# Kernel optimization log

Hardware: AMD Instinct MI355X
Metric: run time of the kernel (lower is better)

## Reference

```python
import jax, jax.numpy as jnp
import numpy as np


def _dct2(x):
    """DCT-II over last dim, scipy norm=None scaling (matches the torch rfft trick:
    X_k = 2 * sum_n x_n cos(pi*k*(2n+1)/(2N))). Expressed as one batched matmul."""
    N = x.shape[-1]
    n = jnp.arange(N, dtype=x.dtype)
    k = jnp.arange(N, dtype=x.dtype)
    # D[k, n] = 2*cos(pi*k*(2n+1)/(2N))
    D = 2.0 * jnp.cos((np.pi / (2.0 * N)) * k[:, None] * (2.0 * n[None, :] + 1.0))
    return jnp.einsum('kn,bcn->bck', D, x)


def setup_inputs() -> dict:
    key = jax.random.key(0)
    k0, k1, k2 = jax.random.split(key, 3)
    b, c, l = 32, 512, 1024
    x = jax.random.normal(k0, (b, c, l), dtype=jnp.float32)
    # 1x1 Conv1d weights (kernel_size=1, bias=False) stored as [out, in]
    w1 = jax.random.normal(k1, (2 * c, c), dtype=jnp.float32) / np.float32(np.sqrt(c))
    w2 = jax.random.normal(k2, (c, 2 * c), dtype=jnp.float32) / np.float32(np.sqrt(2 * c))
    ln_w = jnp.ones((l,), dtype=jnp.float32)
    ln_b = jnp.zeros((l,), dtype=jnp.float32)
    return {"x": x, "w1": w1, "w2": w2, "ln_w": ln_w, "ln_b": ln_b}


def reference(x, w1, w2, ln_w, ln_b):
    eps = 1e-6
    freq = _dct2(x)                                   # [b, c, l]
    mu = jnp.mean(freq, axis=-1, keepdims=True)
    var = jnp.var(freq, axis=-1, keepdims=True)       # biased, like nn.LayerNorm
    h = (freq - mu) * jax.lax.rsqrt(var + eps) * ln_w + ln_b
    # fc: Conv1d(c->2c, k=1) -> Dropout(eval: identity) -> ReLU -> Conv1d(2c->c) -> Sigmoid
    h = jax.nn.relu(jnp.einsum('oi,bil->bol', w1, h))  # [b, 2c, l]
    gate = jax.nn.sigmoid(jnp.einsum('oi,bil->bol', w2, h))  # [b, c, l]
    return x * gate
```

## Files before the change

### kernel.cpp

```cpp
#include <hip/hip_runtime.h>
#include <hip/hip_bf16.h>
#include <math.h>

typedef short short8 __attribute__((ext_vector_type(8)));
typedef short short4v __attribute__((ext_vector_type(4)));
typedef float f32x4 __attribute__((ext_vector_type(4)));

__device__ __forceinline__ short f2bf(float f) {
  union { float f; unsigned u; } v; v.f = f;
  unsigned r = v.u + 0x7FFFu + ((v.u >> 16) & 1u);
  return (short)(r >> 16);
}
__device__ __forceinline__ float bf2f(short s) {
  union { unsigned u; float f; } v; v.u = ((unsigned)(unsigned short)s) << 16;
  return v.f;
}

__global__ __launch_bounds__(256) void cast_kernel(const float* __restrict__ in,
                                                   short* __restrict__ out, int n4) {
  int i = blockIdx.x * blockDim.x + threadIdx.x;
  if (i < n4) {
    float4 v = ((const float4*)in)[i];
    short4v o;
    o.x = f2bf(v.x); o.y = f2bf(v.y); o.z = f2bf(v.z); o.w = f2bf(v.w);
    ((short4v*)out)[i] = o;
  }
}

__global__ __launch_bounds__(256) void prep_eo(const float* __restrict__ x,
                                               short* __restrict__ eo) {
  int t = blockIdx.x * 256 + threadIdx.x;
  int bc = t >> 7, n0 = (t & 127) * 4;
  const float* xr = x + (size_t)bc * 1024;
  float4 f = *(const float4*)(xr + n0);
  float4 r = *(const float4*)(xr + 1020 - n0);
  short4v ef, of;
  ef.x = f2bf(f.x + r.w); ef.y = f2bf(f.y + r.z); ef.z = f2bf(f.z + r.y); ef.w = f2bf(f.w + r.x);
  of.x = f2bf(f.x - r.w); of.y = f2bf(f.y - r.z); of.z = f2bf(f.z - r.y); of.w = f2bf(f.w - r.x);
  *(short4v*)&eo[(size_t)bc * 512 + n0] = ef;
  *(short4v*)&eo[8388608 + (size_t)bc * 512 + n0] = of;
}

__global__ __launch_bounds__(256) void build_Deo(short* __restrict__ D) {
  int t = blockIdx.x * 256 + threadIdx.x;
  int parity = t >> 18, rem = t & 262143;
  int k2 = rem >> 9, n = rem & 511;
  const float s = 1.5339807878856412e-03f;
  float arg = (s * (float)(2 * k2 + parity)) * (float)(2 * n + 1);
  D[t] = f2bf(2.0f * cosf(arg));
}

__global__ __launch_bounds__(256) void ln_stats(const float2* __restrict__ partial,
                                                float2* __restrict__ musd) {
  int n = blockIdx.x * 256 + threadIdx.x;
  float S = 0.f, Q = 0.f;
#pragma unroll
  for (int r = 0; r < 4; ++r) {
    float2 p = partial[(size_t)r * 16384 + n];
    S += p.x; Q += p.y;
  }
  float mu  = S * (1.f / 1024.f);
  float var = Q * (1.f / 1024.f) - mu * mu;
  float2 o; o.x = mu; o.y = rsqrtf(var + 1e-6f);
  musd[n] = o;
}

__global__ __launch_bounds__(256) void ln_apply(short* __restrict__ freqT,
                                                const float2* __restrict__ musd,
                                                const float* __restrict__ lnw,
                                                const float* __restrict__ lnb) {
  int t = blockIdx.x * 256 + threadIdx.x;
  int c8 = t & 63;
  int k  = (t >> 6) & 1023;
  int b  = t >> 16;
  size_t idx = ((size_t)b << 19) + (size_t)k * 512 + (size_t)c8 * 8;
  short8 v = *(const short8*)&freqT[idx];
  float w  = lnw[k];
  float bb = lnb[k];
  const float2* ms = &musd[b * 512 + c8 * 8];
  short8 o;
#pragma unroll
  for (int j = 0; j < 8; ++j) {
    float f = bf2f(v[j]);
    float2 m = ms[j];
    o[j] = f2bf((f - m.x) * m.y * w + bb);
  }
  *(short8*)&freqT[idx] = o;
}

template<int EPI>
__global__ __launch_bounds__(256, 2) void gemmF(
    const short* __restrict__ A, const short* __restrict__ B,
    void* __restrict__ Cout, const float* __restrict__ X,
    float2* __restrict__ P, int K, int NT, long strideA, long strideB)
{
  __shared__ short As[2][8192];
  __shared__ short Bs[2][4096];
  const int tid = threadIdx.x;
  const int l   = tid & 63;
  const int w   = tid >> 6;
  const int wm  = w >> 1;
  const int wc  = w & 1;
  const int lr  = l & 15;
  const int lhi = l >> 4;

  const int nwg = gridDim.x, q = nwg >> 3, orig = blockIdx.x;
  const int wgid = (orig & 7) * q + (orig >> 3);
  int bx, by, bz;
  if (EPI == 0)      { bx = wgid & 1; bz = (wgid >> 1) & 1; by = wgid >> 2; }
  else if (EPI == 1) { by = wgid & 7; bx = (wgid >> 3) & 3; bz = wgid >> 5; }
  else               { bx = wgid & 1; by = (wgid >> 1) & 7; bz = wgid >> 4; }

  const long row0 = (long)bx * 256, col0 = (long)by * 128;
  const short* Ab = A + (size_t)bz * strideA + (size_t)row0 * K;
  const short* Bb = B + (size_t)bz * strideB + (size_t)col0 * K;

  const int sx    = (lhi ^ ((lr >> 1) & 3)) * 8;
  const int abase = (wm * 128 + lr) * 32;
  const int bbase = (wc * 64  + lr) * 32;

  f32x4 acc[8][4];
#pragma unroll
  for (int i = 0; i < 8; ++i)
#pragma unroll
    for (int j = 0; j < 4; ++j) acc[i][j] = (f32x4){0.f, 0.f, 0.f, 0.f};

#define GLL(SRC, DST) __builtin_amdgcn_global_load_lds(                      \
      (const __attribute__((address_space(1))) void*)(SRC),                  \
      (__attribute__((address_space(3))) void*)(DST), 16, 0, 0)

#define STAGE(KT, D) do {                                                    \
    const size_t kb_ = (size_t)(KT) * 32;                                    \
    _Pragma("unroll")                                                        \
    for (int r_ = 0; r_ < 4; ++r_) {                                         \
      int c_ = r_ * 256 + tid; int row_ = c_ >> 2; int sl_ = c_ & 3;         \
      int sc_ = (sl_ ^ ((row_ >> 1) & 3)) * 8;                               \
      GLL(Ab + (size_t)row_ * K + kb_ + sc_, &As[D][row_ * 32 + sl_ * 8]);   \
    }                                                                        \
    _Pragma("unroll")                                                        \
    for (int r_ = 0; r_ < 2; ++r_) {                                         \
      int c_ = r_ * 256 + tid; int row_ = c_ >> 2; int sl_ = c_ & 3;         \
      int sc_ = (sl_ ^ ((row_ >> 1) & 3)) * 8;                               \
      GLL(Bb + (size_t)row_ * K + kb_ + sc_, &Bs[D][row_ * 32 + sl_ * 8]);   \
    }                                                                        \
  } while (0)

#define LD8(PTR, OFF) (*(const short8*)&(PTR)[OFF])
#define MFMA(AV, BV, C) __builtin_amdgcn_mfma_f32_16x16x32_bf16(AV, BV, C, 0, 0, 0)
#define SBAR __builtin_amdgcn_s_barrier()
#define SCHB __builtin_amdgcn_sched_barrier(0)

#define MROW(MI, AV)                                                         \
    acc[MI][0] = MFMA(AV, b0, acc[MI][0]);                                   \
    acc[MI][1] = MFMA(AV, b1, acc[MI][1]);                                   \
    acc[MI][2] = MFMA(AV, b2, acc[MI][2]);                                   \
    acc[MI][3] = MFMA(AV, b3, acc[MI][3]);

  STAGE(0, 0);
  STAGE(1, 1);

  int cur = 0;
  for (int kt = 0; kt < NT; ++kt) {
    if (kt + 1 < NT) { asm volatile("s_waitcnt vmcnt(6)" ::: "memory"); }
    else             { asm volatile("s_waitcnt vmcnt(0)" ::: "memory"); }
    SCHB; SBAR;
    const short* Ad = As[cur];
    const short* Bd = Bs[cur];
    short8 a0, a1, a2, a3, a4, a5, a6, a7, b0, b1, b2, b3;
    a0 = LD8(Ad, abase + 0 * 512 + sx);
    a1 = LD8(Ad, abase + 1 * 512 + sx);
    b0 = LD8(Bd, bbase + 0 * 512 + sx);
    b1 = LD8(Bd, bbase + 1 * 512 + sx);
    b2 = LD8(Bd, bbase + 2 * 512 + sx);
    b3 = LD8(Bd, bbase + 3 * 512 + sx);
    a2 = LD8(Ad, abase + 2 * 512 + sx);
    a3 = LD8(Ad, abase + 3 * 512 + sx);
    a4 = LD8(Ad, abase + 4 * 512 + sx);
    a5 = LD8(Ad, abase + 5 * 512 + sx);
    a6 = LD8(Ad, abase + 6 * 512 + sx);
    a7 = LD8(Ad, abase + 7 * 512 + sx);
    SCHB;
    asm volatile("s_waitcnt lgkmcnt(6)" ::: "memory");
    SCHB;
    __builtin_amdgcn_s_setprio(1);
    MROW(0, a0) MROW(1, a1)
    __builtin_amdgcn_s_setprio(0);
    SCHB;
    asm volatile("s_waitcnt lgkmcnt(0)" ::: "memory");
    SCHB; SBAR;
    if (kt + 2 < NT) STAGE(kt + 2, cur);
    SCHB;
    __builtin_amdgcn_s_setprio(1);
    MROW(2, a2) MROW(3, a3) MROW(4, a4) MROW(5, a5) MROW(6, a6) MROW(7, a7)
    __builtin_amdgcn_s_setprio(0);
    SCHB;
    cur ^= 1;
  }

  float sv[4], qv[4];
#pragma unroll
  for (int ni = 0; ni < 4; ++ni) { sv[ni] = 0.f; qv[ni] = 0.f; }

#pragma unroll
  for (int mi = 0; mi < 8; ++mi) {
#pragma unroll
    for (int ni = 0; ni < 4; ++ni) {
#pragma unroll
      for (int j = 0; j < 4; ++j) {
        int r  = (int)row0 + wm * 128 + mi * 16 + lhi * 4 + j;
        int cc = (int)col0 + wc * 64 + ni * 16 + lr;
        float v = acc[mi][ni][j];
        if (EPI == 0) {
          sv[ni] += v; qv[ni] += v * v;
          int rr = r * 2 + bz;
          ((short*)Cout)[((size_t)(cc >> 9) << 19) + (size_t)rr * 512 + (cc & 511)] = f2bf(v);
        } else if (EPI == 1) {
          ((short*)Cout)[(size_t)bz * 1048576 + (size_t)r * 1024 + cc] = f2bf(v > 0.f ? v : 0.f);
        } else {
          size_t idx = (size_t)bz * 524288 + (size_t)r * 1024 + cc;
          float g = 1.f / (1.f + __expf(-v));
          ((float*)Cout)[idx] = X[idx] * g;
        }
      }
    }
  }

  if (EPI == 0) {
    __syncthreads();
    float* redS = (float*)&As[0][0];
    float* redQ = redS + 1024;
    const int contrib = wm * 4 + lhi;
#pragma unroll
    for (int ni = 0; ni < 4; ++ni) {
      int ccl = wc * 64 + ni * 16 + lr;
      redS[ccl * 8 + contrib] = sv[ni];
      redQ[ccl * 8 + contrib] = qv[ni];
    }
    __syncthreads();
    if (tid < 128) {
      float S = 0.f, Q = 0.f;
#pragma unroll
      for (int i = 0; i < 8; ++i) { S += redS[tid * 8 + i]; Q += redQ[tid * 8 + i]; }
      float2 o; o.x = S; o.y = Q;
      P[(size_t)(bz * 2 + bx) * 16384 + col0 + tid] = o;
    }
  }
#undef MROW
#undef MFMA
#undef LD8
#undef STAGE
#undef GLL
#undef SBAR
#undef SCHB
}

extern "C" void kernel_launch(void* const* d_in, const int* in_sizes, int n_in,
                              void* d_out, int out_size, void* d_ws, size_t ws_size,
                              hipStream_t stream) {
  const float* x    = (const float*)d_in[0];
  const float* w1   = (const float*)d_in[1];
  const float* w2   = (const float*)d_in[2];
  const float* ln_w = (const float*)d_in[3];
  const float* ln_b = (const float*)d_in[4];
  float* out = (float*)d_out;

  char* ws = (char*)d_ws;
  short* Deo    = (short*)(ws);
  short* w1_bf  = (short*)(ws + 1048576);
  short* w2_bf  = (short*)(ws + 2097152);
  short* freqT  = (short*)(ws + 3145728);
  short* z1t    = (short*)(ws + 36700160);
  short* eo     = z1t;
  float2* part  = (float2*)(ws + 103809024);
  float2* musd  = (float2*)(ws + 104857600);

  prep_eo<<<dim3(8192), dim3(256), 0, stream>>>(x, eo);
  cast_kernel<<<dim3(512), dim3(256), 0, stream>>>(w1, w1_bf, 524288 / 4);
  cast_kernel<<<dim3(512), dim3(256), 0, stream>>>(w2, w2_bf, 524288 / 4);
  build_Deo<<<dim3(2048), dim3(256), 0, stream>>>(Deo);

  gemmF<0><<<dim3(512), dim3(256), 0, stream>>>(
      Deo, eo, (void*)freqT, nullptr, part, 512, 16, 262144, 8388608);

  ln_stats<<<dim3(64), dim3(256), 0, stream>>>(part, musd);

  ln_apply<<<dim3(8192), dim3(256), 0, stream>>>(freqT, musd, ln_w, ln_b);

  gemmF<1><<<dim3(1024), dim3(256), 0, stream>>>(
      freqT, w1_bf, (void*)z1t, nullptr, nullptr, 512, 16, 524288, 0);

  gemmF<2><<<dim3(512), dim3(256), 0, stream>>>(
      w2_bf, z1t, (void*)out, x, nullptr, 1024, 32, 0, 1048576);
}
```

Measured before the change: 159.1 us.

## Compute LayerNorm stats analytically from input and fuse normalize into DCT GEMM epilogue

Computes the DCT-domain mean as a dot product of x with a precomputed column-sum vector, and the variance through Parseval-style identities on x. This moves the statistics into prep_eo and lets the first GEMM epilogue apply LayerNorm directly. It removes the partial-stat reduction, the ln_stats kernel and the separate ln_apply read-modify-write pass over the bf16 freq tensor. In exchange it adds two tiny kernels that build the cosine-sum vector, and stats computed in fp32 from x rather than from the bf16-rounded GEMM output.

```diff
diff --git a/kernel.cpp b/kernel.cpp
--- a/kernel.cpp
+++ b/kernel.cpp
@@ -27,8 +27,27 @@
   }
 }
 
+__global__ __launch_bounds__(256) void vbuild(float* __restrict__ vpart) {
+  int t = blockIdx.x * 256 + threadIdx.x;
+  int n = t & 1023, ch = t >> 10;
+  float coef = 1.5339807878856412e-03f * (float)(2 * n + 1);
+  float s = 0.f;
+  for (int k = ch * 128; k < ch * 128 + 128; ++k) s += cosf(coef * (float)k);
+  vpart[(size_t)ch * 1024 + n] = 2.f * s;
+}
+__global__ __launch_bounds__(256) void vfold(const float* __restrict__ vpart,
+                                             float* __restrict__ v) {
+  int n = blockIdx.x * 256 + threadIdx.x;
+  float s = 0.f;
+#pragma unroll
+  for (int r = 0; r < 8; ++r) s += vpart[r * 1024 + n];
+  v[n] = s;
+}
+
 __global__ __launch_bounds__(256) void prep_eo(const float* __restrict__ x,
-                                               short* __restrict__ eo) {
+                                               const float* __restrict__ v,
+                                               short* __restrict__ eo,
+                                               float2* __restrict__ musd) {
   int t = blockIdx.x * 256 + threadIdx.x;
   int bc = t >> 7, n0 = (t & 127) * 4;
   const float* xr = x + (size_t)bc * 1024;
@@ -39,6 +58,36 @@
   of.x = f2bf(f.x - r.w); of.y = f2bf(f.y - r.z); of.z = f2bf(f.z - r.y); of.w = f2bf(f.w - r.x);
   *(short4v*)&eo[(size_t)bc * 512 + n0] = ef;
   *(short4v*)&eo[8388608 + (size_t)bc * 512 + n0] = of;
+
+  float4 vf = *(const float4*)(v + n0);
+  float4 vr = *(const float4*)(v + 1020 - n0);
+  float s2 = f.x*f.x + f.y*f.y + f.z*f.z + f.w*f.w
+           + r.x*r.x + r.y*r.y + r.z*r.z + r.w*r.w;
+  float sx = f.x + f.y + f.z + f.w + r.x + r.y + r.z + r.w;
+  float dt = f.x*vf.x + f.y*vf.y + f.z*vf.z + f.w*vf.w
+           + r.x*vr.x + r.y*vr.y + r.z*vr.z + r.w*vr.w;
+#pragma unroll
+  for (int m = 1; m <= 32; m <<= 1) {
+    s2 += __shfl_xor(s2, m);
+    sx += __shfl_xor(sx, m);
+    dt += __shfl_xor(dt, m);
+  }
+  __shared__ float red[2][2][4];
+  int rowh = threadIdx.x >> 7, wv = (threadIdx.x >> 6) & 1;
+  if ((threadIdx.x & 63) == 0) {
+    red[rowh][wv][0] = s2; red[rowh][wv][1] = sx; red[rowh][wv][2] = dt;
+  }
+  __syncthreads();
+  if ((threadIdx.x & 127) == 0) {
+    float S2 = red[rowh][0][0] + red[rowh][1][0];
+    float SX = red[rowh][0][1] + red[rowh][1][1];
+    float DT = red[rowh][0][2] + red[rowh][1][2];
+    float mu  = DT * (1.f / 1024.f);
+    float ex2 = 2.f * S2 + SX * SX * (1.f / 512.f);
+    float var = ex2 - mu * mu;
+    float2 o; o.x = mu; o.y = rsqrtf(var + 1e-6f);
+    musd[bc] = o;
+  }
 }
 
 __global__ __launch_bounds__(256) void build_Deo(short* __restrict__ D) {
@@ -50,49 +99,13 @@
   D[t] = f2bf(2.0f * cosf(arg));
 }
 
-__global__ __launch_bounds__(256) void ln_stats(const float2* __restrict__ partial,
-                                                float2* __restrict__ musd) {
-  int n = blockIdx.x * 256 + threadIdx.x;
-  float S = 0.f, Q = 0.f;
-#pragma unroll
-  for (int r = 0; r < 4; ++r) {
-    float2 p = partial[(size_t)r * 16384 + n];
-    S += p.x; Q += p.y;
-  }
-  float mu  = S * (1.f / 1024.f);
-  float var = Q * (1.f / 1024.f) - mu * mu;
-  float2 o; o.x = mu; o.y = rsqrtf(var + 1e-6f);
-  musd[n] = o;
-}
-
-__global__ __launch_bounds__(256) void ln_apply(short* __restrict__ freqT,
-                                                const float2* __restrict__ musd,
-                                                const float* __restrict__ lnw,
-                                                const float* __restrict__ lnb) {
-  int t = blockIdx.x * 256 + threadIdx.x;
-  int c8 = t & 63;
-  int k  = (t >> 6) & 1023;
-  int b  = t >> 16;
-  size_t idx = ((size_t)b << 19) + (size_t)k * 512 + (size_t)c8 * 8;
-  short8 v = *(const short8*)&freqT[idx];
-  float w  = lnw[k];
-  float bb = lnb[k];
-  const float2* ms = &musd[b * 512 + c8 * 8];
-  short8 o;
-#pragma unroll
-  for (int j = 0; j < 8; ++j) {
-    float f = bf2f(v[j]);
-    float2 m = ms[j];
-    o[j] = f2bf((f - m.x) * m.y * w + bb);
-  }
-  *(short8*)&freqT[idx] = o;
-}
-
 template<int EPI>
 __global__ __launch_bounds__(256, 2) void gemmF(
     const short* __restrict__ A, const short* __restrict__ B,
     void* __restrict__ Cout, const float* __restrict__ X,
-    float2* __restrict__ P, int K, int NT, long strideA, long strideB)
+    const float2* __restrict__ MS, const float* __restrict__ LNW,
+    const float* __restrict__ LNB,
+    int K, int NT, long strideA, long strideB)
 {
   __shared__ short As[2][8192];
   __shared__ short Bs[2][4096];
@@ -197,23 +210,21 @@
     cur ^= 1;
   }
 
-  float sv[4], qv[4];
-#pragma unroll
-  for (int ni = 0; ni < 4; ++ni) { sv[ni] = 0.f; qv[ni] = 0.f; }
-
 #pragma unroll
   for (int mi = 0; mi < 8; ++mi) {
 #pragma unroll
     for (int ni = 0; ni < 4; ++ni) {
+      int cc = (int)col0 + wc * 64 + ni * 16 + lr;
+      float2 ms;
+      if (EPI == 0) ms = MS[cc];
 #pragma unroll
       for (int j = 0; j < 4; ++j) {
         int r  = (int)row0 + wm * 128 + mi * 16 + lhi * 4 + j;
-        int cc = (int)col0 + wc * 64 + ni * 16 + lr;
         float v = acc[mi][ni][j];
         if (EPI == 0) {
-          sv[ni] += v; qv[ni] += v * v;
           int rr = r * 2 + bz;
-          ((short*)Cout)[((size_t)(cc >> 9) << 19) + (size_t)rr * 512 + (cc & 511)] = f2bf(v);
+          float h = (v - ms.x) * ms.y * LNW[rr] + LNB[rr];
+          ((short*)Cout)[((size_t)(cc >> 9) << 19) + (size_t)rr * 512 + (cc & 511)] = f2bf(h);
         } else if (EPI == 1) {
           ((short*)Cout)[(size_t)bz * 1048576 + (size_t)r * 1024 + cc] = f2bf(v > 0.f ? v : 0.f);
         } else {
@@ -224,27 +235,6 @@
       }
     }
   }
-
-  if (EPI == 0) {
-    __syncthreads();
-    float* redS = (float*)&As[0][0];
-    float* redQ = redS + 1024;
-    const int contrib = wm * 4 + lhi;
-#pragma unroll
-    for (int ni = 0; ni < 4; ++ni) {
-      int ccl = wc * 64 + ni * 16 + lr;
-      redS[ccl * 8 + contrib] = sv[ni];
-      redQ[ccl * 8 + contrib] = qv[ni];
-    }
-    __syncthreads();
-    if (tid < 128) {
-      float S = 0.f, Q = 0.f;
-#pragma unroll
-      for (int i = 0; i < 8; ++i) { S += redS[tid * 8 + i]; Q += redQ[tid * 8 + i]; }
-      float2 o; o.x = S; o.y = Q;
-      P[(size_t)(bz * 2 + bx) * 16384 + col0 + tid] = o;
-    }
-  }
 #undef MROW
 #undef MFMA
 #undef LD8
@@ -271,24 +261,23 @@
   short* freqT  = (short*)(ws + 3145728);
   short* z1t    = (short*)(ws + 36700160);
   short* eo     = z1t;
-  float2* part  = (float2*)(ws + 103809024);
+  float* vpart  = (float*)(ws + 103809024);
+  float* vvec   = (float*)(ws + 103874560);
   float2* musd  = (float2*)(ws + 104857600);
 
-  prep_eo<<<dim3(8192), dim3(256), 0, stream>>>(x, eo);
+  vbuild<<<dim3(32), dim3(256), 0, stream>>>(vpart);
+  vfold<<<dim3(4), dim3(256), 0, stream>>>(vpart, vvec);
+  prep_eo<<<dim3(8192), dim3(256), 0, stream>>>(x, vvec, eo, musd);
   cast_kernel<<<dim3(512), dim3(256), 0, stream>>>(w1, w1_bf, 524288 / 4);
   cast_kernel<<<dim3(512), dim3(256), 0, stream>>>(w2, w2_bf, 524288 / 4);
   build_Deo<<<dim3(2048), dim3(256), 0, stream>>>(Deo);
 
   gemmF<0><<<dim3(512), dim3(256), 0, stream>>>(
-      Deo, eo, (void*)freqT, nullptr, part, 512, 16, 262144, 8388608);
-
-  ln_stats<<<dim3(64), dim3(256), 0, stream>>>(part, musd);
-
-  ln_apply<<<dim3(8192), dim3(256), 0, stream>>>(freqT, musd, ln_w, ln_b);
+      Deo, eo, (void*)freqT, nullptr, musd, ln_w, ln_b, 512, 16, 262144, 8388608);
 
   gemmF<1><<<dim3(1024), dim3(256), 0, stream>>>(
-      freqT, w1_bf, (void*)z1t, nullptr, nullptr, 512, 16, 524288, 0);
+      freqT, w1_bf, (void*)z1t, nullptr, nullptr, nullptr, nullptr, 512, 16, 524288, 0);
 
   gemmF<2><<<dim3(512), dim3(256), 0, stream>>>(
-      w2_bf, z1t, (void*)out, x, nullptr, 1024, 32, 0, 1048576);
-}
+      w2_bf, z1t, (void*)out, x, nullptr, nullptr, nullptr, 1024, 32, 0, 1048576);
+}
```

After: 168.8 us. 1.06x slower.
